# Performance work log

Hardware: AMD Instinct MI355X
Metric: run time of the kernel (lower is better)

## Reference

```python
import jax, jax.numpy as jnp
import numpy as np

HEADS = 8
DIM_HEAD = 32
SCALE = DIM_HEAD ** -0.5
EPS = 1e-12  # F.normalize eps


def _rmsnorm_ch(t, g):
    # F.normalize(t, dim=1) * g * sqrt(C)  (normalize_dim=1)
    c = t.shape[1]
    norm = jnp.sqrt(jnp.sum(t * t, axis=1, keepdims=True))
    return t / jnp.maximum(norm, EPS) * g[None, :, None, None] * (c ** 0.5)


def setup_inputs() -> dict:
    key = jax.random.key(0)
    ks = jax.random.split(key, 4)
    B, C, H, W = 16, 256, 64, 64
    hidden = HEADS * DIM_HEAD  # 256
    x = jax.random.normal(ks[0], (B, C, H, W), dtype=jnp.float32)
    g1 = jnp.ones((C,), dtype=jnp.float32)
    # conv 1x1 weights stored as [out_ch, in_ch]
    w_qkv = jax.random.normal(ks[1], (hidden * 3, C), dtype=jnp.float32) * (1.0 / np.sqrt(C))
    w_out = jax.random.normal(ks[2], (C, hidden), dtype=jnp.float32) * (1.0 / np.sqrt(hidden))
    b_out = jnp.zeros((C,), dtype=jnp.float32)
    g2 = jnp.ones((C,), dtype=jnp.float32)
    return {"x": x, "g1": g1, "w_qkv": w_qkv, "w_out": w_out, "b_out": b_out, "g2": g2}


def reference(x, g1, w_qkv, w_out, b_out, g2):
    b, c, h, w = x.shape
    n = h * w
    xn = _rmsnorm_ch(x, g1)
    # 1x1 conv (no bias) == channel matmul
    qkv = jnp.einsum('oc,bchw->bohw', w_qkv, xn)
    q, k, v = jnp.split(qkv, 3, axis=1)
    # b (h c) x y -> b h c (x y)
    q = q.reshape(b, HEADS, DIM_HEAD, n)
    k = k.reshape(b, HEADS, DIM_HEAD, n)
    v = v.reshape(b, HEADS, DIM_HEAD, n)
    q = jax.nn.softmax(q, axis=-2) * SCALE  # softmax over dim_head
    k = jax.nn.softmax(k, axis=-1)          # softmax over sequence
    context = jnp.einsum('bhdn,bhen->bhde', k, v)  # [b,h,d,e] small
    out = jnp.einsum('bhde,bhdn->bhen', context, q)
    out = out.reshape(b, HEADS * DIM_HEAD, h, w)
    out = jnp.einsum('oc,bchw->bohw', w_out, out) + b_out[None, :, None, None]
    return _rmsnorm_ch(out, g2) + x
```

## Files before the change

### kernel.cpp

```cpp
#include <hip/hip_runtime.h>
#include <math.h>


#define B_ 16
#define C_ 256
#define N_ 4096
#define SCALE_ 0.17677669529663687f
#define EPS_ 1e-12f

typedef __attribute__((ext_vector_type(8))) short bf16x8;
typedef __attribute__((ext_vector_type(4))) float f32x4;

__device__ __forceinline__ ushort f2bf(float f) {
    union { float f; uint u; } x; x.f = f;
    uint r = (x.u + 0x7FFFu + ((x.u >> 16) & 1u)) >> 16;
    return (ushort)r;
}
__device__ __forceinline__ float bf2f(ushort s) {
    union { uint u; float f; } x; x.u = ((uint)s) << 16;
    return x.f;
}

__global__ __launch_bounds__(256) void k_prep(const float* __restrict__ w_qkv,
                                              const float* __restrict__ g1,
                                              ushort* __restrict__ Wp) {
    int o = blockIdx.x, c = threadIdx.x;
    Wp[(size_t)o * 256 + c] = f2bf(w_qkv[(size_t)o * 256 + c] * g1[c]);
}

__global__ __launch_bounds__(256) void k_xconv(const float* __restrict__ x,
                                               ushort* __restrict__ xnbT) {
    __shared__ float ssp[4][64];
    __shared__ float rinv_s[64];
    __shared__ ushort T[64][268];
    int b = blockIdx.y, n0 = blockIdx.x * 64;
    const float* xb = x + (size_t)b * C_ * N_ + n0;
    int t = threadIdx.x;
    int nl = t & 63, cg = t >> 6;
    float ss = 0.f;
    #pragma unroll 8
    for (int i = 0; i < 64; ++i) {
        float v = xb[(size_t)(cg * 64 + i) * N_ + nl];
        ss += v * v;
    }
    ssp[cg][nl] = ss;
    __syncthreads();
    if (t < 64)
        rinv_s[t] = 16.f / fmaxf(sqrtf(ssp[0][t] + ssp[1][t] + ssp[2][t] + ssp[3][t]), EPS_);
    __syncthreads();
    float rv = rinv_s[nl];
    #pragma unroll 8
    for (int i = 0; i < 64; ++i) {
        int c = cg * 64 + i;
        T[nl][c] = f2bf(xb[(size_t)c * N_ + nl] * rv);
    }
    __syncthreads();
    int j = t >> 2, ch = t & 3;
    ushort* orow = xnbT + ((size_t)b * N_ + n0 + j) * 256 + ch * 64;
    #pragma unroll
    for (int i = 0; i < 8; ++i)
        *(uint2*)&orow[i * 8] = *(const uint2*)&T[j][ch * 64 + i * 8],
        *(uint2*)&orow[i * 8 + 4] = *(const uint2*)&T[j][ch * 64 + i * 8 + 4];
}

__global__ __launch_bounds__(256) void k_gemm(const ushort* __restrict__ Wp,
                                              const ushort* __restrict__ xnbT,
                                              ushort* __restrict__ kvOut,
                                              ushort* __restrict__ qTOut,
                                              int qmode) {
    __shared__ ushort Asub[128][40];
    __shared__ ushort Bsub[128][40];
    const int b = blockIdx.z;
    const int wrow0 = (qmode ? 0 : 256) + blockIdx.y * 128;
    const int col0 = blockIdx.x * 128;
    const int t = threadIdx.x;
    const int l = t & 63, w = t >> 6;
    const int wr = w >> 1, wc = w & 1, grp = l >> 4;
    const ushort* xb = xnbT + (size_t)b * N_ * 256;
    f32x4 acc[4][4] = {};

    for (int k0 = 0; k0 < 256; k0 += 32) {
        int r = t >> 1, ko = (t & 1) * 16;
        const uint4* sa = (const uint4*)(Wp + (size_t)(wrow0 + r) * 256 + k0 + ko);
        *(uint4*)&Asub[r][ko]     = sa[0];
        *(uint4*)&Asub[r][ko + 8] = sa[1];
        const uint4* sb = (const uint4*)(xb + (size_t)(col0 + r) * 256 + k0 + ko);
        *(uint4*)&Bsub[r][ko]     = sb[0];
        *(uint4*)&Bsub[r][ko + 8] = sb[1];
        __syncthreads();
        bf16x8 af[4], bfv[4];
        #pragma unroll
        for (int m = 0; m < 4; ++m)
            af[m] = *(const bf16x8*)&Asub[wr * 64 + m * 16 + (l & 15)][grp * 8];
        #pragma unroll
        for (int n = 0; n < 4; ++n)
            bfv[n] = *(const bf16x8*)&Bsub[wc * 64 + n * 16 + (l & 15)][grp * 8];
        #pragma unroll
        for (int m = 0; m < 4; ++m)
            #pragma unroll
            for (int n = 0; n < 4; ++n)
                acc[m][n] = __builtin_amdgcn_mfma_f32_16x16x32_bf16(af[m], bfv[n], acc[m][n], 0, 0, 0);
        __syncthreads();
    }

    if (qmode) {
        ushort* qTb = qTOut + (size_t)b * N_ * 256;
        #pragma unroll
        for (int n = 0; n < 4; ++n) {
            int cg = col0 + wc * 64 + n * 16 + (l & 15);
            float f[4][4];
            #pragma unroll
            for (int m = 0; m < 4; ++m)
                #pragma unroll
                for (int r = 0; r < 4; ++r) f[m][r] = acc[m][n][r];
            float mxA = -1e30f, mxB = -1e30f;
            #pragma unroll
            for (int r = 0; r < 4; ++r) {
                mxA = fmaxf(mxA, fmaxf(f[0][r], f[1][r]));
                mxB = fmaxf(mxB, fmaxf(f[2][r], f[3][r]));
            }
            mxA = fmaxf(mxA, __shfl_xor(mxA, 16));
            mxA = fmaxf(mxA, __shfl_xor(mxA, 32));
            mxB = fmaxf(mxB, __shfl_xor(mxB, 16));
            mxB = fmaxf(mxB, __shfl_xor(mxB, 32));
            float sA = 0.f, sB = 0.f;
            #pragma unroll
            for (int r = 0; r < 4; ++r) {
                f[0][r] = __expf(f[0][r] - mxA); sA += f[0][r];
                f[1][r] = __expf(f[1][r] - mxA); sA += f[1][r];
                f[2][r] = __expf(f[2][r] - mxB); sB += f[2][r];
                f[3][r] = __expf(f[3][r] - mxB); sB += f[3][r];
            }
            sA += __shfl_xor(sA, 16); sA += __shfl_xor(sA, 32);
            sB += __shfl_xor(sB, 16); sB += __shfl_xor(sB, 32);
            float iA = 1.f / sA, iB = 1.f / sB;
            #pragma unroll
            for (int m = 0; m < 4; ++m) {
                float sc = (m < 2) ? iA : iB;
                int rbase = wrow0 + wr * 64 + m * 16 + grp * 4;
                uint2 pk;
                pk.x = (uint)f2bf(f[m][0] * sc) | ((uint)f2bf(f[m][1] * sc) << 16);
                pk.y = (uint)f2bf(f[m][2] * sc) | ((uint)f2bf(f[m][3] * sc) << 16);
                *(uint2*)&qTb[(size_t)cg * 256 + rbase] = pk;
            }
        }
    } else {
        ushort* kvb = kvOut + (size_t)b * 512 * N_;
        #pragma unroll
        for (int n = 0; n < 4; ++n) {
            int cg = col0 + wc * 64 + n * 16 + (l & 15);
            #pragma unroll
            for (int m = 0; m < 4; ++m) {
                int rbase = wrow0 - 256 + wr * 64 + m * 16 + grp * 4;
                #pragma unroll
                for (int r = 0; r < 4; ++r)
                    kvb[(size_t)(rbase + r) * N_ + cg] = f2bf(acc[m][n][r]);
            }
        }
    }
}

__global__ __launch_bounds__(256) void k_ctxpart(const ushort* __restrict__ kv,
                                                 float* __restrict__ ctxp,
                                                 float* __restrict__ sums_p) {
    __shared__ float red[4][32][33];
    __shared__ float redp[4][32];
    int bh = blockIdx.x, s = blockIdx.y;
    int b = bh >> 3, h = bh & 7;
    int t = threadIdx.x, l = t & 63, w = t >> 6;
    const ushort* kb = kv + (size_t)b * 512 * N_ + (size_t)(h * 32) * N_;
    const ushort* vb = kv + (size_t)b * 512 * N_ + (size_t)(256 + h * 32) * N_;
    const int n0base = s * 1024 + w * 256;
    const int row = l & 15, grp = l >> 4;
    f32x4 acc[2][2] = {};
    float psA = 0.f, psB = 0.f;

    for (int it = 0; it < 8; ++it) {
        int n0 = n0base + it * 32 + grp * 8;
        bf16x8 k0 = *(const bf16x8*)&kb[(size_t)row * N_ + n0];
        bf16x8 k1 = *(const bf16x8*)&kb[(size_t)(row + 16) * N_ + n0];
        bf16x8 v0 = *(const bf16x8*)&vb[(size_t)row * N_ + n0];
        bf16x8 v1 = *(const bf16x8*)&vb[(size_t)(row + 16) * N_ + n0];
        bf16x8 p0, p1;
        #pragma unroll
        for (int j = 0; j < 8; ++j) {
            ushort r0 = f2bf(__expf(bf2f((ushort)k0[j])));
            ushort r1 = f2bf(__expf(bf2f((ushort)k1[j])));
            p0[j] = (short)r0; p1[j] = (short)r1;
            psA += bf2f(r0); psB += bf2f(r1);
        }
        acc[0][0] = __builtin_amdgcn_mfma_f32_16x16x32_bf16(p0, v0, acc[0][0], 0, 0, 0);
        acc[0][1] = __builtin_amdgcn_mfma_f32_16x16x32_bf16(p0, v1, acc[0][1], 0, 0, 0);
        acc[1][0] = __builtin_amdgcn_mfma_f32_16x16x32_bf16(p1, v0, acc[1][0], 0, 0, 0);
        acc[1][1] = __builtin_amdgcn_mfma_f32_16x16x32_bf16(p1, v1, acc[1][1], 0, 0, 0);
    }

    psA += __shfl_xor(psA, 16); psA += __shfl_xor(psA, 32);
    psB += __shfl_xor(psB, 16); psB += __shfl_xor(psB, 32);
    #pragma unroll
    for (int mi = 0; mi < 2; ++mi)
        #pragma unroll
        for (int ni = 0; ni < 2; ++ni)
            #pragma unroll
            for (int r = 0; r < 4; ++r)
                red[w][mi * 16 + grp * 4 + r][ni * 16 + row] = acc[mi][ni][r];
    if (l < 16) { redp[w][l] = psA; redp[w][16 + l] = psB; }
    __syncthreads();

    size_t base = (size_t)(s * 128 + bh) * 32;
    #pragma unroll
    for (int i = t; i < 1024; i += 256) {
        int d = i >> 5, e = i & 31;
        ctxp[(base + d) * 32 + e] =
            red[0][d][e] + red[1][d][e] + red[2][d][e] + red[3][d][e];
    }
    if (t < 32)
        sums_p[base + t] = redp[0][t] + redp[1][t] + redp[2][t] + redp[3][t];
}

__global__ __launch_bounds__(256) void k_fold(const float* __restrict__ w_out,
                                              const float* __restrict__ ctxp,
                                              const float* __restrict__ sums_p,
                                              ushort* __restrict__ M) {
    __shared__ float cn[32][33];
    __shared__ float sinv[32];
    int bh = blockIdx.x;
    int b = bh >> 3, h = bh & 7;
    int t = threadIdx.x;
    if (t < 32) {
        float st = 0.f;
        #pragma unroll
        for (int s = 0; s < 4; ++s) st += sums_p[(size_t)(s * 128 + bh) * 32 + t];
        sinv[t] = SCALE_ / st;
    }
    #pragma unroll
    for (int i = t; i < 1024; i += 256) {
        int d = i >> 5, e = i & 31;
        float cv = 0.f;
        #pragma unroll
        for (int s = 0; s < 4; ++s)
            cv += ctxp[((size_t)(s * 128 + bh) * 32 + d) * 32 + e];
        cn[e][d] = cv;
    }
    __syncthreads();
    float wreg[32];
    const float* wr = w_out + (size_t)t * 256 + h * 32;
    #pragma unroll
    for (int e = 0; e < 32; e += 4) {
        float4 wv = *(const float4*)&wr[e];
        wreg[e] = wv.x; wreg[e + 1] = wv.y; wreg[e + 2] = wv.z; wreg[e + 3] = wv.w;
    }
    float acc[32] = {};
    #pragma unroll
    for (int e = 0; e < 32; ++e) {
        float we = wreg[e];
        #pragma unroll
        for (int d = 0; d < 32; ++d) acc[d] += we * cn[e][d];
    }
    ushort* Mrow = M + ((size_t)b * 256 + t) * 256 + h * 32;
    #pragma unroll
    for (int d = 0; d < 32; ++d) Mrow[d] = f2bf(acc[d] * sinv[d]);
}

__global__ __launch_bounds__(512) void k_final(const ushort* __restrict__ M,
                                               const ushort* __restrict__ qT,
                                               const float* __restrict__ b_out,
                                               const float* __restrict__ g2,
                                               const float* __restrict__ x,
                                               float* __restrict__ out) {
    __shared__ ushort Asub[256][40];
    __shared__ ushort Bsub[128][40];
    __shared__ float ss2[4][128];
    int b = blockIdx.y;
    int col0 = blockIdx.x * 128;
    int t = threadIdx.x, l = t & 63, w = t >> 6;
    int wr = w >> 1, wc = w & 1;
    const ushort* Mb = M + (size_t)b * 256 * 256;
    const ushort* qTb = qT + (size_t)b * N_ * 256;
    f32x4 acc[4][4] = {};

    for (int k0 = 0; k0 < 256; k0 += 32) {
        {
            int r = t >> 1, ko = (t & 1) * 16;
            const uint4* src = (const uint4*)(Mb + (size_t)r * 256 + k0 + ko);
            *(uint4*)&Asub[r][ko]     = src[0];
            *(uint4*)&Asub[r][ko + 8] = src[1];
        }
        {
            int nl = t & 127, ko = (t >> 7) * 8;
            *(uint4*)&Bsub[nl][ko] =
                *(const uint4*)(qTb + (size_t)(col0 + nl) * 256 + k0 + ko);
        }
        __syncthreads();
        bf16x8 af[4], bfv[4];
        #pragma unroll
        for (int m = 0; m < 4; ++m)
            af[m] = *(const bf16x8*)&Asub[wr * 64 + m * 16 + (l & 15)][(l >> 4) * 8];
        #pragma unroll
        for (int n = 0; n < 4; ++n)
            bfv[n] = *(const bf16x8*)&Bsub[wc * 64 + n * 16 + (l & 15)][(l >> 4) * 8];
        #pragma unroll
        for (int m = 0; m < 4; ++m)
            #pragma unroll
            for (int n = 0; n < 4; ++n)
                acc[m][n] = __builtin_amdgcn_mfma_f32_16x16x32_bf16(af[m], bfv[n], acc[m][n], 0, 0, 0);
        __syncthreads();
    }

    #pragma unroll
    for (int n = 0; n < 4; ++n) {
        float local = 0.f;
        #pragma unroll
        for (int m = 0; m < 4; ++m) {
            int obase = wr * 64 + m * 16 + (l >> 4) * 4;
            #pragma unroll
            for (int r = 0; r < 4; ++r) {
                float f = acc[m][n][r] + b_out[obase + r];
                acc[m][n][r] = f;
                local += f * f;
            }
        }
        local += __shfl_xor(local, 16);
        local += __shfl_xor(local, 32);
        if ((l >> 4) == 0) ss2[wr][wc * 64 + n * 16 + (l & 15)] = local;
    }
    __syncthreads();
    const float* xb = x + (size_t)b * C_ * N_;
    float* ob = out + (size_t)b * C_ * N_;
    #pragma unroll
    for (int n = 0; n < 4; ++n) {
        int cl = wc * 64 + n * 16 + (l & 15);
        int cg = col0 + cl;
        float tot = ss2[0][cl] + ss2[1][cl] + ss2[2][cl] + ss2[3][cl];
        float rs = 16.f / fmaxf(sqrtf(tot), EPS_);
        #pragma unroll
        for (int m = 0; m < 4; ++m) {
            int obase = wr * 64 + m * 16 + (l >> 4) * 4;
            #pragma unroll
            for (int r = 0; r < 4; ++r) {
                int o = obase + r;
                ob[(size_t)o * N_ + cg] = acc[m][n][r] * rs * g2[o] + xb[(size_t)o * N_ + cg];
            }
        }
    }
}

extern "C" void kernel_launch(void* const* d_in, const int* in_sizes, int n_in,
                              void* d_out, int out_size, void* d_ws, size_t ws_size,
                              hipStream_t stream) {
    const float* x     = (const float*)d_in[0];
    const float* g1    = (const float*)d_in[1];
    const float* w_qkv = (const float*)d_in[2];
    const float* w_out = (const float*)d_in[3];
    const float* b_out = (const float*)d_in[4];
    const float* g2    = (const float*)d_in[5];
    float* out = (float*)d_out;
    char* ws = (char*)d_ws;

    ushort* Wp     = (ushort*)(ws + 0);
    float*  ctxp   = (float*)(ws + 393216);
    float*  sums_p = (float*)(ws + 2490368);
    ushort* Mm     = (ushort*)(ws + 2555904);
    ushort* xnbT   = (ushort*)(ws + 4653056);
    ushort* kv     = (ushort*)(ws + 38207488);
    ushort* qT     = kv;

    k_prep<<<768, 256, 0, stream>>>(w_qkv, g1, Wp);
    k_xconv<<<dim3(64, 16), 256, 0, stream>>>(x, xnbT);
    k_gemm<<<dim3(32, 4, 16), 256, 0, stream>>>(Wp, xnbT, kv, nullptr, 0);
    k_ctxpart<<<dim3(128, 4), 256, 0, stream>>>(kv, ctxp, sums_p);
    k_fold<<<128, 256, 0, stream>>>(w_out, ctxp, sums_p, Mm);
    k_gemm<<<dim3(32, 2, 16), 256, 0, stream>>>(Wp, xnbT, nullptr, qT, 1);
    k_final<<<dim3(32, 16), 512, 0, stream>>>(Mm, qT, b_out, g2, x, out);
}
```

Before: 160.7 us.

## Fuse q projection and softmax into final output GEMM via LDS

```diff
diff --git a/kernel.cpp b/kernel.cpp
--- a/kernel.cpp
+++ b/kernel.cpp
@@ -65,13 +65,11 @@
 
 __global__ __launch_bounds__(256) void k_gemm(const ushort* __restrict__ Wp,
                                               const ushort* __restrict__ xnbT,
-                                              ushort* __restrict__ kvOut,
-                                              ushort* __restrict__ qTOut,
-                                              int qmode) {
+                                              ushort* __restrict__ kvOut) {
     __shared__ ushort Asub[128][40];
     __shared__ ushort Bsub[128][40];
     const int b = blockIdx.z;
-    const int wrow0 = (qmode ? 0 : 256) + blockIdx.y * 128;
+    const int wrow0 = 256 + blockIdx.y * 128;
     const int col0 = blockIdx.x * 128;
     const int t = threadIdx.x;
     const int l = t & 63, w = t >> 6;
@@ -103,59 +101,16 @@
         __syncthreads();
     }
 
-    if (qmode) {
-        ushort* qTb = qTOut + (size_t)b * N_ * 256;
-        #pragma unroll
-        for (int n = 0; n < 4; ++n) {
-            int cg = col0 + wc * 64 + n * 16 + (l & 15);
-            float f[4][4];
-            #pragma unroll
-            for (int m = 0; m < 4; ++m)
-                #pragma unroll
-                for (int r = 0; r < 4; ++r) f[m][r] = acc[m][n][r];
-            float mxA = -1e30f, mxB = -1e30f;
-            #pragma unroll
-            for (int r = 0; r < 4; ++r) {
-                mxA = fmaxf(mxA, fmaxf(f[0][r], f[1][r]));
-                mxB = fmaxf(mxB, fmaxf(f[2][r], f[3][r]));
-            }
-            mxA = fmaxf(mxA, __shfl_xor(mxA, 16));
-            mxA = fmaxf(mxA, __shfl_xor(mxA, 32));
-            mxB = fmaxf(mxB, __shfl_xor(mxB, 16));
-            mxB = fmaxf(mxB, __shfl_xor(mxB, 32));
-            float sA = 0.f, sB = 0.f;
-            #pragma unroll
-            for (int r = 0; r < 4; ++r) {
-                f[0][r] = __expf(f[0][r] - mxA); sA += f[0][r];
-                f[1][r] = __expf(f[1][r] - mxA); sA += f[1][r];
-                f[2][r] = __expf(f[2][r] - mxB); sB += f[2][r];
-                f[3][r] = __expf(f[3][r] - mxB); sB += f[3][r];
-            }
-            sA += __shfl_xor(sA, 16); sA += __shfl_xor(sA, 32);
-            sB += __shfl_xor(sB, 16); sB += __shfl_xor(sB, 32);
-            float iA = 1.f / sA, iB = 1.f / sB;
-            #pragma unroll
-            for (int m = 0; m < 4; ++m) {
-                float sc = (m < 2) ? iA : iB;
-                int rbase = wrow0 + wr * 64 + m * 16 + grp * 4;
-                uint2 pk;
-                pk.x = (uint)f2bf(f[m][0] * sc) | ((uint)f2bf(f[m][1] * sc) << 16);
-                pk.y = (uint)f2bf(f[m][2] * sc) | ((uint)f2bf(f[m][3] * sc) << 16);
-                *(uint2*)&qTb[(size_t)cg * 256 + rbase] = pk;
-            }
-        }
-    } else {
-        ushort* kvb = kvOut + (size_t)b * 512 * N_;
-        #pragma unroll
-        for (int n = 0; n < 4; ++n) {
-            int cg = col0 + wc * 64 + n * 16 + (l & 15);
-            #pragma unroll
-            for (int m = 0; m < 4; ++m) {
-                int rbase = wrow0 - 256 + wr * 64 + m * 16 + grp * 4;
-                #pragma unroll
-                for (int r = 0; r < 4; ++r)
-                    kvb[(size_t)(rbase + r) * N_ + cg] = f2bf(acc[m][n][r]);
-            }
+    ushort* kvb = kvOut + (size_t)b * 512 * N_;
+    #pragma unroll
+    for (int n = 0; n < 4; ++n) {
+        int cg = col0 + wc * 64 + n * 16 + (l & 15);
+        #pragma unroll
+        for (int m = 0; m < 4; ++m) {
+            int rbase = wrow0 - 256 + wr * 64 + m * 16 + grp * 4;
+            #pragma unroll
+            for (int r = 0; r < 4; ++r)
+                kvb[(size_t)(rbase + r) * N_ + cg] = f2bf(acc[m][n][r]);
         }
     }
 }
@@ -262,45 +217,43 @@
     for (int d = 0; d < 32; ++d) Mrow[d] = f2bf(acc[d] * sinv[d]);
 }
 
-__global__ __launch_bounds__(512) void k_final(const ushort* __restrict__ M,
-                                               const ushort* __restrict__ qT,
-                                               const float* __restrict__ b_out,
-                                               const float* __restrict__ g2,
-                                               const float* __restrict__ x,
-                                               float* __restrict__ out) {
+__global__ __launch_bounds__(512) void k_qfinal(const ushort* __restrict__ Wp,
+                                                const ushort* __restrict__ xnbT,
+                                                const ushort* __restrict__ M,
+                                                const float* __restrict__ b_out,
+                                                const float* __restrict__ g2,
+                                                const float* __restrict__ x,
+                                                float* __restrict__ out) {
     __shared__ ushort Asub[256][40];
-    __shared__ ushort Bsub[128][40];
-    __shared__ float ss2[4][128];
-    int b = blockIdx.y;
-    int col0 = blockIdx.x * 128;
-    int t = threadIdx.x, l = t & 63, w = t >> 6;
-    int wr = w >> 1, wc = w & 1;
-    const ushort* Mb = M + (size_t)b * 256 * 256;
-    const ushort* qTb = qT + (size_t)b * N_ * 256;
-    f32x4 acc[4][4] = {};
+    __shared__ ushort Bsub[64][40];
+    __shared__ ushort qlds[64 * 256];
+    __shared__ float ss2[8][64];
+    const int b = blockIdx.y, col0 = blockIdx.x * 64;
+    const int t = threadIdx.x, l = t & 63, w = t >> 6;
+    const int lr = l & 15, grp = l >> 4;
+    const ushort* xb = xnbT + (size_t)b * N_ * 256;
+    f32x4 acc[2][4] = {};
 
     for (int k0 = 0; k0 < 256; k0 += 32) {
-        {
-            int r = t >> 1, ko = (t & 1) * 16;
-            const uint4* src = (const uint4*)(Mb + (size_t)r * 256 + k0 + ko);
-            *(uint4*)&Asub[r][ko]     = src[0];
-            *(uint4*)&Asub[r][ko + 8] = src[1];
-        }
-        {
-            int nl = t & 127, ko = (t >> 7) * 8;
-            *(uint4*)&Bsub[nl][ko] =
-                *(const uint4*)(qTb + (size_t)(col0 + nl) * 256 + k0 + ko);
-        }
-        __syncthreads();
-        bf16x8 af[4], bfv[4];
-        #pragma unroll
-        for (int m = 0; m < 4; ++m)
-            af[m] = *(const bf16x8*)&Asub[wr * 64 + m * 16 + (l & 15)][(l >> 4) * 8];
+        { int r = t >> 1, ko = (t & 1) * 16;
+          const uint4* sa = (const uint4*)(Wp + (size_t)r * 256 + k0 + ko);
+          *(uint4*)&Asub[r][ko]     = sa[0];
+          *(uint4*)&Asub[r][ko + 8] = sa[1]; }
+        if (t < 128) {
+          int r = t >> 1, ko = (t & 1) * 16;
+          const uint4* sb = (const uint4*)(xb + (size_t)(col0 + r) * 256 + k0 + ko);
+          *(uint4*)&Bsub[r][ko]     = sb[0];
+          *(uint4*)&Bsub[r][ko + 8] = sb[1]; }
+        __syncthreads();
+        bf16x8 af[2], bfv[4];
+        #pragma unroll
+        for (int m = 0; m < 2; ++m)
+            af[m] = *(const bf16x8*)&Asub[w * 32 + m * 16 + lr][grp * 8];
         #pragma unroll
         for (int n = 0; n < 4; ++n)
-            bfv[n] = *(const bf16x8*)&Bsub[wc * 64 + n * 16 + (l & 15)][(l >> 4) * 8];
-        #pragma unroll
-        for (int m = 0; m < 4; ++m)
+            bfv[n] = *(const bf16x8*)&Bsub[n * 16 + lr][grp * 8];
+        #pragma unroll
+        for (int m = 0; m < 2; ++m)
             #pragma unroll
             for (int n = 0; n < 4; ++n)
                 acc[m][n] = __builtin_amdgcn_mfma_f32_16x16x32_bf16(af[m], bfv[n], acc[m][n], 0, 0, 0);
@@ -309,37 +262,96 @@
 
     #pragma unroll
     for (int n = 0; n < 4; ++n) {
+        float f[2][4];
+        #pragma unroll
+        for (int m = 0; m < 2; ++m)
+            #pragma unroll
+            for (int r = 0; r < 4; ++r) f[m][r] = acc[m][n][r];
+        float mx = -1e30f;
+        #pragma unroll
+        for (int r = 0; r < 4; ++r) mx = fmaxf(mx, fmaxf(f[0][r], f[1][r]));
+        mx = fmaxf(mx, __shfl_xor(mx, 16));
+        mx = fmaxf(mx, __shfl_xor(mx, 32));
+        float s = 0.f;
+        #pragma unroll
+        for (int r = 0; r < 4; ++r) {
+            f[0][r] = __expf(f[0][r] - mx); s += f[0][r];
+            f[1][r] = __expf(f[1][r] - mx); s += f[1][r];
+        }
+        s += __shfl_xor(s, 16); s += __shfl_xor(s, 32);
+        float inv = 1.f / s;
+        int cl = n * 16 + lr;
+        #pragma unroll
+        for (int m = 0; m < 2; ++m) {
+            int d = w * 32 + m * 16 + grp * 4;
+            uint2 pk;
+            pk.x = (uint)f2bf(f[m][0] * inv) | ((uint)f2bf(f[m][1] * inv) << 16);
+            pk.y = (uint)f2bf(f[m][2] * inv) | ((uint)f2bf(f[m][3] * inv) << 16);
+            uint off = (uint)(cl * 512 + d * 2) ^ (uint)((cl & 7) << 4);
+            *(uint2*)((char*)qlds + off) = pk;
+        }
+    }
+
+    f32x4 acc2[2][4] = {};
+    const ushort* Mb = M + (size_t)b * 256 * 256;
+    for (int k0 = 0; k0 < 256; k0 += 32) {
+        { int r = t >> 1, ko = (t & 1) * 16;
+          const uint4* sa = (const uint4*)(Mb + (size_t)r * 256 + k0 + ko);
+          *(uint4*)&Asub[r][ko]     = sa[0];
+          *(uint4*)&Asub[r][ko + 8] = sa[1]; }
+        __syncthreads();
+        bf16x8 af[2], bq[4];
+        #pragma unroll
+        for (int m = 0; m < 2; ++m)
+            af[m] = *(const bf16x8*)&Asub[w * 32 + m * 16 + lr][grp * 8];
+        #pragma unroll
+        for (int n = 0; n < 4; ++n) {
+            int row = n * 16 + lr;
+            uint off = (uint)(row * 512 + (k0 + grp * 8) * 2) ^ (uint)((row & 7) << 4);
+            bq[n] = *(const bf16x8*)((const char*)qlds + off);
+        }
+        #pragma unroll
+        for (int m = 0; m < 2; ++m)
+            #pragma unroll
+            for (int n = 0; n < 4; ++n)
+                acc2[m][n] = __builtin_amdgcn_mfma_f32_16x16x32_bf16(af[m], bq[n], acc2[m][n], 0, 0, 0);
+        __syncthreads();
+    }
+
+    #pragma unroll
+    for (int n = 0; n < 4; ++n) {
         float local = 0.f;
         #pragma unroll
-        for (int m = 0; m < 4; ++m) {
-            int obase = wr * 64 + m * 16 + (l >> 4) * 4;
+        for (int m = 0; m < 2; ++m) {
+            int obase = w * 32 + m * 16 + grp * 4;
             #pragma unroll
             for (int r = 0; r < 4; ++r) {
-                float f = acc[m][n][r] + b_out[obase + r];
-                acc[m][n][r] = f;
+                float f = acc2[m][n][r] + b_out[obase + r];
+                acc2[m][n][r] = f;
                 local += f * f;
             }
         }
         local += __shfl_xor(local, 16);
         local += __shfl_xor(local, 32);
-        if ((l >> 4) == 0) ss2[wr][wc * 64 + n * 16 + (l & 15)] = local;
-    }
-    __syncthreads();
-    const float* xb = x + (size_t)b * C_ * N_;
+        if (grp == 0) ss2[w][n * 16 + lr] = local;
+    }
+    __syncthreads();
+    const float* xb2 = x + (size_t)b * C_ * N_;
     float* ob = out + (size_t)b * C_ * N_;
     #pragma unroll
     for (int n = 0; n < 4; ++n) {
-        int cl = wc * 64 + n * 16 + (l & 15);
+        int cl = n * 16 + lr;
         int cg = col0 + cl;
-        float tot = ss2[0][cl] + ss2[1][cl] + ss2[2][cl] + ss2[3][cl];
+        float tot = ss2[0][cl] + ss2[1][cl] + ss2[2][cl] + ss2[3][cl]
+                  + ss2[4][cl] + ss2[5][cl] + ss2[6][cl] + ss2[7][cl];
         float rs = 16.f / fmaxf(sqrtf(tot), EPS_);
         #pragma unroll
-        for (int m = 0; m < 4; ++m) {
-            int obase = wr * 64 + m * 16 + (l >> 4) * 4;
+        for (int m = 0; m < 2; ++m) {
+            int obase = w * 32 + m * 16 + grp * 4;
             #pragma unroll
             for (int r = 0; r < 4; ++r) {
                 int o = obase + r;
-                ob[(size_t)o * N_ + cg] = acc[m][n][r] * rs * g2[o] + xb[(size_t)o * N_ + cg];
+                ob[(size_t)o * N_ + cg] = acc2[m][n][r] * rs * g2[o] + xb2[(size_t)o * N_ + cg];
             }
         }
     }
@@ -363,13 +375,11 @@
     ushort* Mm     = (ushort*)(ws + 2555904);
     ushort* xnbT   = (ushort*)(ws + 4653056);
     ushort* kv     = (ushort*)(ws + 38207488);
-    ushort* qT     = kv;
 
     k_prep<<<768, 256, 0, stream>>>(w_qkv, g1, Wp);
     k_xconv<<<dim3(64, 16), 256, 0, stream>>>(x, xnbT);
-    k_gemm<<<dim3(32, 4, 16), 256, 0, stream>>>(Wp, xnbT, kv, nullptr, 0);
+    k_gemm<<<dim3(32, 4, 16), 256, 0, stream>>>(Wp, xnbT, kv);
     k_ctxpart<<<dim3(128, 4), 256, 0, stream>>>(kv, ctxp, sums_p);
     k_fold<<<128, 256, 0, stream>>>(w_out, ctxp, sums_p, Mm);
-    k_gemm<<<dim3(32, 2, 16), 256, 0, stream>>>(Wp, xnbT, nullptr, qT, 1);
-    k_final<<<dim3(32, 16), 512, 0, stream>>>(Mm, qT, b_out, g2, x, out);
-}
+    k_qfinal<<<dim3(64, 16), 512, 0, stream>>>(Wp, xnbT, Mm, b_out, g2, x, out);
+}
```

Result: faster. 152.3 us (-5.2%).
